# Kernel tuning notes

Measured on AMD Instinct MI355X. Metric: run time of the kernel, lower is better.

## Reference

```python
import jax, jax.numpy as jnp
import numpy as np

INPUT_SIZE = 63
HIDDEN = 128
NUM_CLASSES = 11
B, T = 4096, 128


def _gru_layer(x_seq, w_ih, w_hh, b_ih, b_hh):
    """PyTorch-semantics GRU layer. x_seq: [B,T,D] -> outputs [B,T,H]."""
    Bsz = x_seq.shape[0]
    H = w_hh.shape[1]
    # Precompute input projections for all timesteps in one big GEMM: [B,T,3H]
    gates_x = jnp.einsum('btd,gd->btg', x_seq, w_ih) + b_ih

    def step(h, gx):
        gh = h @ w_hh.T + b_hh                       # [B,3H]
        xr, xz, xn = jnp.split(gx, 3, axis=-1)
        hr, hz, hn = jnp.split(gh, 3, axis=-1)
        r = jax.nn.sigmoid(xr + hr)
        z = jax.nn.sigmoid(xz + hz)
        n = jnp.tanh(xn + r * hn)
        h_new = (1.0 - z) * n + z * h
        return h_new, h_new

    h0 = jnp.zeros((Bsz, H), x_seq.dtype)
    _, ys = jax.lax.scan(step, h0, jnp.swapaxes(gates_x, 0, 1))  # ys: [T,B,H]
    return jnp.swapaxes(ys, 0, 1)


def setup_inputs() -> dict:
    key = jax.random.key(0)
    ks = jax.random.split(key, 13)
    s_ih0 = 1.0 / np.sqrt(HIDDEN)
    u = lambda k, shape, s: jax.random.uniform(k, shape, jnp.float32, -s, s)
    inp = {
        'x': jax.random.normal(ks[0], (B, T, INPUT_SIZE), jnp.float32),
        # GRU layer 0: input_size=63 -> hidden=128
        'w_ih0': u(ks[1], (3 * HIDDEN, INPUT_SIZE), s_ih0),
        'w_hh0': u(ks[2], (3 * HIDDEN, HIDDEN), s_ih0),
        'b_ih0': u(ks[3], (3 * HIDDEN,), s_ih0),
        'b_hh0': u(ks[4], (3 * HIDDEN,), s_ih0),
        # GRU layer 1: hidden -> hidden
        'w_ih1': u(ks[5], (3 * HIDDEN, HIDDEN), s_ih0),
        'w_hh1': u(ks[6], (3 * HIDDEN, HIDDEN), s_ih0),
        'b_ih1': u(ks[7], (3 * HIDDEN,), s_ih0),
        'b_hh1': u(ks[8], (3 * HIDDEN,), s_ih0),
        # classifier: Linear(128,64) -> ReLU -> Linear(64,11)
        'w1': u(ks[9], (64, HIDDEN), 1.0 / np.sqrt(HIDDEN)),
        'b1': u(ks[10], (64,), 1.0 / np.sqrt(HIDDEN)),
        'w2': u(ks[11], (NUM_CLASSES, 64), 1.0 / np.sqrt(64)),
        'b2': u(ks[12], (NUM_CLASSES,), 1.0 / np.sqrt(64)),
    }
    return inp


def reference(x, w_ih0, w_hh0, b_ih0, b_hh0, w_ih1, w_hh1, b_ih1, b_hh1, w1, b1, w2, b2):
    h1 = _gru_layer(x, w_ih0, w_hh0, b_ih0, b_hh0)    # [B,T,H]
    h2 = _gru_layer(h1, w_ih1, w_hh1, b_ih1, b_hh1)   # [B,T,H]
    last = h2[:, -1, :]                               # [B,H]
    hidden = jax.nn.relu(last @ w1.T + b1)            # [B,64] (dropout is identity in eval)
    return hidden @ w2.T + b2                         # [B,num_classes]
```

## Files before the change

### kernel.cpp

```cpp
#include <hip/hip_runtime.h>
#include <hip/hip_bf16.h>

typedef __attribute__((ext_vector_type(8))) short s8v;
typedef __attribute__((ext_vector_type(4))) float f4v;

#define MF(A, B, C) C = __builtin_amdgcn_mfma_f32_16x16x32_bf16((A), (B), (C), 0, 0, 0)

__device__ __forceinline__ ushort f2bf(float f) {
  unsigned u = __float_as_uint(f);
  u += 0x7FFF + ((u >> 16) & 1);
  return (ushort)(u >> 16);
}
__device__ __forceinline__ float bf2f(ushort h) {
  return __uint_as_float(((unsigned)h) << 16);
}
__device__ __forceinline__ float sigm(float p) { return 1.f / (1.f + __expf(-p)); }
__device__ __forceinline__ float tanh_safe(float a) {
  float t = __expf(-2.f * fabsf(a));
  float ng = (1.f - t) / (1.f + t);
  return a < 0.f ? -ng : ng;
}
__device__ __forceinline__ float dot4(float4 a, float4 b) {
  return fmaf(a.x, b.x, fmaf(a.y, b.y, fmaf(a.z, b.z, a.w * b.w)));
}

__global__ void conv_x(const float* __restrict__ x, ushort* __restrict__ xhi,
                       ushort* __restrict__ xlo, int total) {
  int idx = blockIdx.x * 256 + threadIdx.x;
  if (idx >= total) return;
  int k4 = (idx & 15) * 4;
  long bt = idx >> 4;
  #pragma unroll
  for (int j = 0; j < 4; ++j) {
    int k = k4 + j;
    float v = (k < 63) ? x[bt * 63 + k] : 0.f;
    ushort hi = f2bf(v);
    xhi[bt * 64 + k] = hi;
    xlo[bt * 64 + k] = f2bf(v - bf2f(hi));
  }
}

__global__ void pack_fr(const float* __restrict__ src, ushort* __restrict__ dst,
                        int Kreal, int KT, int total) {
  int idx = blockIdx.x * 256 + threadIdx.x;
  if (idx >= total) return;
  int i = idx & 7, l = (idx >> 3) & 63, hl = (idx >> 9) & 1;
  int rest = idx >> 10;
  int kt = rest % KT, nt = rest / KT;
  int g = nt * 16 + (l & 15);
  int k = kt * 32 + (l >> 4) * 8 + i;
  float v = (k < Kreal) ? src[g * Kreal + k] : 0.f;
  ushort hi = f2bf(v);
  dst[idx] = hl ? f2bf(v - bf2f(hi)) : hi;
}

__global__ void __attribute__((amdgpu_flat_work_group_size(512, 512),
                               amdgpu_waves_per_eu(2, 2)))
rec_l0(const ushort* __restrict__ xhi, const ushort* __restrict__ xlo,
       const ushort* __restrict__ fih, const ushort* __restrict__ fhh,
       const float* __restrict__ bi, const float* __restrict__ bh,
       ushort* __restrict__ s_hi, ushort* __restrict__ s_lo,
       ushort* __restrict__ c_hi, ushort* __restrict__ c_lo,
       int t0, int tc, int first)
{
  __shared__ __align__(16) ushort hh_[2][2048], hl_[2][2048];
  __shared__ __align__(16) float bb[512];
  const int tid = threadIdx.x;
  const int l = tid & 63, wv = tid >> 6;
  const int lr = l & 15, lg = l >> 4;
  const long b0 = (long)blockIdx.x * 16;

  if (tid < 128) {
    bb[tid]       = bi[tid] + bh[tid];
    bb[128 + tid] = bi[128 + tid] + bh[128 + tid];
    bb[256 + tid] = bi[256 + tid];
    bb[384 + tid] = bh[256 + tid];
  }
  const int u0 = (wv << 4) + (lg << 2);
  const int hb = lr * 256 + ((u0 << 1) ^ ((lr & 7) << 4));
  if (first) {
    *(ushort4*)((char*)hh_[0] + hb) = make_ushort4(0, 0, 0, 0);
    *(ushort4*)((char*)hl_[0] + hb) = make_ushort4(0, 0, 0, 0);
  } else {
    *(ushort4*)((char*)hh_[0] + hb) = *(const ushort4*)&c_hi[(b0 + lr) * 128 + u0];
    *(ushort4*)((char*)hl_[0] + hb) = *(const ushort4*)&c_lo[(b0 + lr) * 128 + u0];
  }

  s8v Ba[12];
  s8v Bb[24];
  #pragma unroll
  for (int gi = 0; gi < 3; ++gi) {
    int nt = wv + 8 * gi;
    #pragma unroll
    for (int kt = 0; kt < 2; ++kt)
      #pragma unroll
      for (int hl = 0; hl < 2; ++hl)
        Ba[(gi * 2 + kt) * 2 + hl] = *(const s8v*)&fih[((long)((nt * 2 + kt) * 2 + hl)) * 512 + l * 8];
    #pragma unroll
    for (int kt = 0; kt < 4; ++kt)
      #pragma unroll
      for (int hl = 0; hl < 2; ++hl)
        Bb[(gi * 4 + kt) * 2 + hl] = *(const s8v*)&fhh[((long)((nt * 4 + kt) * 2 + hl)) * 512 + l * 8];
  }

  s8v xch[2], xcl[2], xnh[2], xnl[2];
  {
    long xo = ((b0 + lr) * 128 + t0) * 64 + lg * 8;
    xch[0] = *(const s8v*)&xhi[xo]; xch[1] = *(const s8v*)&xhi[xo + 32];
    xcl[0] = *(const s8v*)&xlo[xo]; xcl[1] = *(const s8v*)&xlo[xo + 32];
  }
  __syncthreads();

  const long sbase = (b0 + lr) * 128 + u0;
  ushort4 st_h, st_l;

  int pp = 0;
  for (int s = 0; s < tc; ++s, pp ^= 1) {
    if (s > 0) {
      *(ushort4*)&s_hi[sbase + (long)(s - 1) * 524288] = st_h;
      *(ushort4*)&s_lo[sbase + (long)(s - 1) * 524288] = st_l;
    }
    if (s + 1 < tc) {
      long xo = ((b0 + lr) * 128 + (t0 + s + 1)) * 64 + lg * 8;
      xnh[0] = *(const s8v*)&xhi[xo]; xnh[1] = *(const s8v*)&xhi[xo + 32];
      xnl[0] = *(const s8v*)&xlo[xo]; xnl[1] = *(const s8v*)&xlo[xo + 32];
    }
    f4v ar = {0.f, 0.f, 0.f, 0.f}, az = ar, anx = ar, anh = ar;
    #pragma unroll
    for (int kt = 0; kt < 4; ++kt) {
      int ba = lr * 256 + ((kt * 64 + lg * 16) ^ ((lr & 7) << 4));
      s8v Ah = *(const s8v*)((const char*)hh_[pp] + ba);
      s8v Al = *(const s8v*)((const char*)hl_[pp] + ba);
      MF(Bb[(0 * 4 + kt) * 2 + 0], Ah, ar);
      MF(Bb[(1 * 4 + kt) * 2 + 0], Ah, az);
      MF(Bb[(2 * 4 + kt) * 2 + 0], Ah, anh);
      MF(Bb[(0 * 4 + kt) * 2 + 1], Ah, ar);
      MF(Bb[(1 * 4 + kt) * 2 + 1], Ah, az);
      MF(Bb[(2 * 4 + kt) * 2 + 1], Ah, anh);
      MF(Bb[(0 * 4 + kt) * 2 + 0], Al, ar);
      MF(Bb[(1 * 4 + kt) * 2 + 0], Al, az);
      MF(Bb[(2 * 4 + kt) * 2 + 0], Al, anh);
    }
    #pragma unroll
    for (int kt = 0; kt < 2; ++kt) {
      MF(Ba[(0 * 2 + kt) * 2 + 0], xch[kt], ar);
      MF(Ba[(1 * 2 + kt) * 2 + 0], xch[kt], az);
      MF(Ba[(2 * 2 + kt) * 2 + 0], xch[kt], anx);
      MF(Ba[(0 * 2 + kt) * 2 + 1], xch[kt], ar);
      MF(Ba[(1 * 2 + kt) * 2 + 1], xch[kt], az);
      MF(Ba[(2 * 2 + kt) * 2 + 1], xch[kt], anx);
      MF(Ba[(0 * 2 + kt) * 2 + 0], xcl[kt], ar);
      MF(Ba[(1 * 2 + kt) * 2 + 0], xcl[kt], az);
      MF(Ba[(2 * 2 + kt) * 2 + 0], xcl[kt], anx);
    }
    {
      ushort4 oh = *(const ushort4*)((const char*)hh_[pp] + hb);
      ushort4 ol = *(const ushort4*)((const char*)hl_[pp] + hb);
      f4v vbr = *(const f4v*)&bb[u0];
      f4v vbz = *(const f4v*)&bb[128 + u0];
      f4v vbx = *(const f4v*)&bb[256 + u0];
      f4v vbh = *(const f4v*)&bb[384 + u0];
      const ushort* ohp = (const ushort*)&oh;
      const ushort* olp = (const ushort*)&ol;
      ushort nh_[4], nl_[4];
      #pragma unroll
      for (int j = 0; j < 4; ++j) {
        float hold = bf2f(ohp[j]) + bf2f(olp[j]);
        float rg = sigm(ar[j] + vbr[j]);
        float zg = sigm(az[j] + vbz[j]);
        float ng = tanh_safe(anx[j] + vbx[j] + rg * (anh[j] + vbh[j]));
        float hn = (1.f - zg) * ng + zg * hold;
        ushort hbf = f2bf(hn);
        nh_[j] = hbf; nl_[j] = f2bf(hn - bf2f(hbf));
      }
      ushort4 wh = make_ushort4(nh_[0], nh_[1], nh_[2], nh_[3]);
      ushort4 wl = make_ushort4(nl_[0], nl_[1], nl_[2], nl_[3]);
      *(ushort4*)((char*)hh_[pp ^ 1] + hb) = wh;
      *(ushort4*)((char*)hl_[pp ^ 1] + hb) = wl;
      st_h = wh; st_l = wl;
    }
    xch[0] = xnh[0]; xch[1] = xnh[1]; xcl[0] = xnl[0]; xcl[1] = xnl[1];
    __syncthreads();
  }
  *(ushort4*)&s_hi[sbase + (long)(tc - 1) * 524288] = st_h;
  *(ushort4*)&s_lo[sbase + (long)(tc - 1) * 524288] = st_l;
  *(ushort4*)&c_hi[(b0 + lr) * 128 + u0] = *(const ushort4*)((const char*)hh_[pp] + hb);
  *(ushort4*)&c_lo[(b0 + lr) * 128 + u0] = *(const ushort4*)((const char*)hl_[pp] + hb);
}

__global__ void __attribute__((amdgpu_flat_work_group_size(512, 512),
                               amdgpu_waves_per_eu(2, 2)))
rec_l1(const ushort* __restrict__ s_hi, const ushort* __restrict__ s_lo,
       const ushort* __restrict__ fih, const ushort* __restrict__ fhh,
       const float* __restrict__ bi, const float* __restrict__ bh,
       ushort* __restrict__ c_hi, ushort* __restrict__ c_lo,
       float* __restrict__ h1f, int tc, int first, int last)
{
  __shared__ __align__(16) ushort hh_[2][2048], hl_[2][2048];
  __shared__ __align__(16) ushort gh_[2][2048], gl_[2][2048];
  __shared__ __align__(16) float bb[512];
  const int tid = threadIdx.x;
  const int l = tid & 63, wv = tid >> 6;
  const int lr = l & 15, lg = l >> 4;
  const long b0 = (long)blockIdx.x * 16;

  if (tid < 128) {
    bb[tid]       = bi[tid] + bh[tid];
    bb[128 + tid] = bi[128 + tid] + bh[128 + tid];
    bb[256 + tid] = bi[256 + tid];
    bb[384 + tid] = bh[256 + tid];
  }
  const int u0 = (wv << 4) + (lg << 2);
  const int hb = lr * 256 + ((u0 << 1) ^ ((lr & 7) << 4));
  if (first) {
    *(ushort4*)((char*)hh_[0] + hb) = make_ushort4(0, 0, 0, 0);
    *(ushort4*)((char*)hl_[0] + hb) = make_ushort4(0, 0, 0, 0);
  } else {
    *(ushort4*)((char*)hh_[0] + hb) = *(const ushort4*)&c_hi[(b0 + lr) * 128 + u0];
    *(ushort4*)((char*)hl_[0] + hb) = *(const ushort4*)&c_lo[(b0 + lr) * 128 + u0];
  }

  const int stid = tid & 255;
  const int srow = stid >> 4, sc16 = stid & 15;
  const int sdst = srow * 256 + ((sc16 * 16) ^ ((srow & 7) << 4));
  const ushort* ssel = (tid < 256) ? s_hi : s_lo;
  ushort* dsel = (tid < 256) ? &gh_[0][0] : &gl_[0][0];

  s8v Ba[24], Bb[24];
  #pragma unroll
  for (int gi = 0; gi < 3; ++gi) {
    int nt = wv + 8 * gi;
    #pragma unroll
    for (int kt = 0; kt < 4; ++kt)
      #pragma unroll
      for (int hl = 0; hl < 2; ++hl) {
        Ba[(gi * 4 + kt) * 2 + hl] = *(const s8v*)&fih[((long)((nt * 4 + kt) * 2 + hl)) * 512 + l * 8];
        Bb[(gi * 4 + kt) * 2 + hl] = *(const s8v*)&fhh[((long)((nt * 4 + kt) * 2 + hl)) * 512 + l * 8];
      }
  }
  {
    s8v v = *(const s8v*)&ssel[((long)0 * 4096 + b0 + srow) * 128 + sc16 * 8];
    *(s8v*)((char*)(dsel + 0 * 2048) + sdst) = v;
  }
  __syncthreads();

  int pp = 0;
  for (int tl = 0; tl < tc; ++tl, pp ^= 1) {
    s8v sreg;
    const int havenext = (tl + 1 < tc);
    if (havenext)
      sreg = *(const s8v*)&ssel[((long)(tl + 1) * 4096 + b0 + srow) * 128 + sc16 * 8];

    f4v ar = {0.f, 0.f, 0.f, 0.f}, az = ar, anx = ar, anh = ar;
    #pragma unroll
    for (int kt = 0; kt < 4; ++kt) {
      int ba = lr * 256 + ((kt * 64 + lg * 16) ^ ((lr & 7) << 4));
      s8v Hh = *(const s8v*)((const char*)hh_[pp] + ba);
      s8v Hl = *(const s8v*)((const char*)hl_[pp] + ba);
      s8v Gh = *(const s8v*)((const char*)gh_[pp] + ba);
      s8v Gl = *(const s8v*)((const char*)gl_[pp] + ba);
      MF(Bb[(0 * 4 + kt) * 2 + 0], Hh, ar);
      MF(Ba[(0 * 4 + kt) * 2 + 0], Gh, ar);
      MF(Bb[(1 * 4 + kt) * 2 + 0], Hh, az);
      MF(Ba[(1 * 4 + kt) * 2 + 0], Gh, az);
      MF(Bb[(2 * 4 + kt) * 2 + 0], Hh, anh);
      MF(Ba[(2 * 4 + kt) * 2 + 0], Gh, anx);
      MF(Bb[(0 * 4 + kt) * 2 + 1], Hh, ar);
      MF(Ba[(0 * 4 + kt) * 2 + 1], Gh, ar);
      MF(Bb[(1 * 4 + kt) * 2 + 1], Hh, az);
      MF(Ba[(1 * 4 + kt) * 2 + 1], Gh, az);
      MF(Bb[(2 * 4 + kt) * 2 + 1], Hh, anh);
      MF(Ba[(2 * 4 + kt) * 2 + 1], Gh, anx);
      MF(Bb[(0 * 4 + kt) * 2 + 0], Hl, ar);
      MF(Ba[(0 * 4 + kt) * 2 + 0], Gl, ar);
      MF(Bb[(1 * 4 + kt) * 2 + 0], Hl, az);
      MF(Ba[(1 * 4 + kt) * 2 + 0], Gl, az);
      MF(Bb[(2 * 4 + kt) * 2 + 0], Hl, anh);
      MF(Ba[(2 * 4 + kt) * 2 + 0], Gl, anx);
    }
    {
      ushort4 oh = *(const ushort4*)((const char*)hh_[pp] + hb);
      ushort4 ol = *(const ushort4*)((const char*)hl_[pp] + hb);
      f4v vbr = *(const f4v*)&bb[u0];
      f4v vbz = *(const f4v*)&bb[128 + u0];
      f4v vbx = *(const f4v*)&bb[256 + u0];
      f4v vbh = *(const f4v*)&bb[384 + u0];
      const ushort* ohp = (const ushort*)&oh;
      const ushort* olp = (const ushort*)&ol;
      ushort nh_[4], nl_[4];
      #pragma unroll
      for (int j = 0; j < 4; ++j) {
        float hold = bf2f(ohp[j]) + bf2f(olp[j]);
        float rg = sigm(ar[j] + vbr[j]);
        float zg = sigm(az[j] + vbz[j]);
        float ng = tanh_safe(anx[j] + vbx[j] + rg * (anh[j] + vbh[j]));
        float hn = (1.f - zg) * ng + zg * hold;
        ushort hbf = f2bf(hn);
        nh_[j] = hbf; nl_[j] = f2bf(hn - bf2f(hbf));
      }
      *(ushort4*)((char*)hh_[pp ^ 1] + hb) = make_ushort4(nh_[0], nh_[1], nh_[2], nh_[3]);
      *(ushort4*)((char*)hl_[pp ^ 1] + hb) = make_ushort4(nl_[0], nl_[1], nl_[2], nl_[3]);
    }
    if (havenext)
      *(s8v*)((char*)(dsel + (size_t)(pp ^ 1) * 2048) + sdst) = sreg;
    __syncthreads();
  }
  {
    ushort4 fh = *(const ushort4*)((const char*)hh_[pp] + hb);
    ushort4 fl = *(const ushort4*)((const char*)hl_[pp] + hb);
    *(ushort4*)&c_hi[(b0 + lr) * 128 + u0] = fh;
    *(ushort4*)&c_lo[(b0 + lr) * 128 + u0] = fl;
    if (last) {
      const ushort* fhp = (const ushort*)&fh;
      const ushort* flp = (const ushort*)&fl;
      float4 o;
      o.x = bf2f(fhp[0]) + bf2f(flp[0]);
      o.y = bf2f(fhp[1]) + bf2f(flp[1]);
      o.z = bf2f(fhp[2]) + bf2f(flp[2]);
      o.w = bf2f(fhp[3]) + bf2f(flp[3]);
      *(float4*)&h1f[(b0 + lr) * 128 + u0] = o;
    }
  }
}

__global__ __launch_bounds__(512) void head_k(
    const float* __restrict__ h1f, const float* __restrict__ w1,
    const float* __restrict__ b1, const float* __restrict__ w2,
    const float* __restrict__ b2, float* __restrict__ out)
{
  __shared__ float hrow[16][132];
  __shared__ float w1s[64][132];
  __shared__ float hid[16][68];
  const int tid = threadIdx.x;
  const long b0 = (long)blockIdx.x * 16;
  for (int i = tid; i < 64 * 128; i += 512) w1s[i >> 7][i & 127] = w1[i];
  {
    int rr = tid >> 5, k4 = (tid & 31) * 4;
    *(float4*)&hrow[rr][k4] = *(const float4*)&h1f[(b0 + rr) * 128 + k4];
  }
  __syncthreads();
  {
    int r = tid & 15, fu = tid >> 4;
    float a0 = 0.f, a1 = 0.f;
    for (int k4 = 0; k4 < 32; ++k4) {
      float4 hv = *(const float4*)&hrow[r][k4 * 4];
      float4 wa = *(const float4*)&w1s[fu][k4 * 4];
      float4 wb = *(const float4*)&w1s[fu + 32][k4 * 4];
      a0 += dot4(wa, hv);
      a1 += dot4(wb, hv);
    }
    a0 += b1[fu]; a1 += b1[fu + 32];
    hid[r][fu]      = fmaxf(a0, 0.f);
    hid[r][fu + 32] = fmaxf(a1, 0.f);
  }
  __syncthreads();
  if (tid < 176) {
    int rr = tid / 11, c = tid - rr * 11;
    float acc = b2[c];
    for (int k = 0; k < 64; ++k) acc = fmaf(w2[c * 64 + k], hid[rr][k], acc);
    out[(b0 + rr) * 11 + c] = acc;
  }
}

extern "C" void kernel_launch(void* const* d_in, const int* in_sizes, int n_in,
                              void* d_out, int out_size, void* d_ws, size_t ws_size,
                              hipStream_t stream) {
  (void)in_sizes; (void)n_in; (void)out_size;
  const float* x    = (const float*)d_in[0];
  const float* wih0 = (const float*)d_in[1];
  const float* whh0 = (const float*)d_in[2];
  const float* bih0 = (const float*)d_in[3];
  const float* bhh0 = (const float*)d_in[4];
  const float* wih1 = (const float*)d_in[5];
  const float* whh1 = (const float*)d_in[6];
  const float* bih1 = (const float*)d_in[7];
  const float* bhh1 = (const float*)d_in[8];
  const float* w1   = (const float*)d_in[9];
  const float* b1   = (const float*)d_in[10];
  const float* w2   = (const float*)d_in[11];
  const float* b2   = (const float*)d_in[12];

  char* wsb = (char*)d_ws;
  size_t o = 0;
  ushort* fih0 = (ushort*)(wsb + o); o += 98304;
  ushort* fhh0 = (ushort*)(wsb + o); o += 196608;
  ushort* fih1 = (ushort*)(wsb + o); o += 196608;
  ushort* fhh1 = (ushort*)(wsb + o); o += 196608;
  ushort* xhi  = (ushort*)(wsb + o); o += 67108864ULL;
  ushort* xlo  = (ushort*)(wsb + o); o += 67108864ULL;
  ushort* hc0h = (ushort*)(wsb + o); o += 1048576;
  ushort* hc0l = (ushort*)(wsb + o); o += 1048576;
  ushort* hc1h = (ushort*)(wsb + o); o += 1048576;
  ushort* hc1l = (ushort*)(wsb + o); o += 1048576;
  float*  h1f  = (float*)(wsb + o);  o += 2097152;

  long rem = (long)ws_size - (long)o;
  long tcmax = rem / (2 * 1048576L);
  int Tc = tcmax > 128 ? 128 : (int)tcmax;
  if (Tc < 1) return;
  ushort* sh = (ushort*)(wsb + o);
  ushort* sl = sh + (long)Tc * 524288;

  hipLaunchKernelGGL(conv_x, dim3(32768), dim3(256), 0, stream, x, xhi, xlo, 8388608);
  hipLaunchKernelGGL(pack_fr, dim3(192), dim3(256), 0, stream, wih0, fih0, 63, 2, 49152);
  hipLaunchKernelGGL(pack_fr, dim3(384), dim3(256), 0, stream, whh0, fhh0, 128, 4, 98304);
  hipLaunchKernelGGL(pack_fr, dim3(384), dim3(256), 0, stream, wih1, fih1, 128, 4, 98304);
  hipLaunchKernelGGL(pack_fr, dim3(384), dim3(256), 0, stream, whh1, fhh1, 128, 4, 98304);

  for (int t0 = 0; t0 < 128; t0 += Tc) {
    int tc = (128 - t0) < Tc ? (128 - t0) : Tc;
    hipLaunchKernelGGL(rec_l0, dim3(256), dim3(512), 0, stream,
                       xhi, xlo, fih0, fhh0, bih0, bhh0, sh, sl, hc0h, hc0l,
                       t0, tc, (int)(t0 == 0));
    hipLaunchKernelGGL(rec_l1, dim3(256), dim3(512), 0, stream,
                       sh, sl, fih1, fhh1, bih1, bhh1, hc1h, hc1l, h1f,
                       tc, (int)(t0 == 0), (int)(t0 + tc == 128));
  }
  hipLaunchKernelGGL(head_k, dim3(256), dim3(512), 0, stream,
                     h1f, w1, b1, w2, b2, (float*)d_out);
}
```

Measured before the change: 652.6 us.

## Prefetch layer-1 inputs via global_load_lds and split MFMA accumulators

In the layer-1 GRU kernel, the next timestep's layer-0 output is now loaded straight into swizzled LDS with global_load_lds, replacing the register round-trip and explicit LDS store. In both recurrent kernels the r and z gate accumulators are split into separate input-path and hidden-path chains, which are summed at the gate. In the layer-0 kernel the input-projection MFMAs are issued before the hidden ones. The split breaks serial MFMA dependency chains so more instructions can be in flight, and the direct-to-LDS load frees registers and VALU work. The risk is the async LDS write ordering relative to the barrier, plus a few extra adds and accumulator registers.

Measured after the change: 703.1 us. +7.7%, slower.

```diff
diff --git a/kernel.cpp b/kernel.cpp
--- a/kernel.cpp
+++ b/kernel.cpp
@@ -22,6 +22,11 @@
 }
 __device__ __forceinline__ float dot4(float4 a, float4 b) {
   return fmaf(a.x, b.x, fmaf(a.y, b.y, fmaf(a.z, b.z, a.w * b.w)));
+}
+__device__ __forceinline__ void glds16(const ushort* g, ushort* l) {
+  __builtin_amdgcn_global_load_lds(
+      (const __attribute__((address_space(1))) unsigned int*)g,
+      (__attribute__((address_space(3))) unsigned int*)l, 16, 0, 0);
 }
 
 __global__ void conv_x(const float* __restrict__ x, ushort* __restrict__ xhi,
@@ -125,33 +130,34 @@
       xnh[0] = *(const s8v*)&xhi[xo]; xnh[1] = *(const s8v*)&xhi[xo + 32];
       xnl[0] = *(const s8v*)&xlo[xo]; xnl[1] = *(const s8v*)&xlo[xo + 32];
     }
-    f4v ar = {0.f, 0.f, 0.f, 0.f}, az = ar, anx = ar, anh = ar;
+    f4v arX = {0.f, 0.f, 0.f, 0.f}, azX = arX, anx = arX;
+    #pragma unroll
+    for (int kt = 0; kt < 2; ++kt) {
+      MF(Ba[(0 * 2 + kt) * 2 + 0], xch[kt], arX);
+      MF(Ba[(1 * 2 + kt) * 2 + 0], xch[kt], azX);
+      MF(Ba[(2 * 2 + kt) * 2 + 0], xch[kt], anx);
+      MF(Ba[(0 * 2 + kt) * 2 + 1], xch[kt], arX);
+      MF(Ba[(1 * 2 + kt) * 2 + 1], xch[kt], azX);
+      MF(Ba[(2 * 2 + kt) * 2 + 1], xch[kt], anx);
+      MF(Ba[(0 * 2 + kt) * 2 + 0], xcl[kt], arX);
+      MF(Ba[(1 * 2 + kt) * 2 + 0], xcl[kt], azX);
+      MF(Ba[(2 * 2 + kt) * 2 + 0], xcl[kt], anx);
+    }
+    f4v arH = {0.f, 0.f, 0.f, 0.f}, azH = arH, anh = arH;
     #pragma unroll
     for (int kt = 0; kt < 4; ++kt) {
       int ba = lr * 256 + ((kt * 64 + lg * 16) ^ ((lr & 7) << 4));
       s8v Ah = *(const s8v*)((const char*)hh_[pp] + ba);
       s8v Al = *(const s8v*)((const char*)hl_[pp] + ba);
-      MF(Bb[(0 * 4 + kt) * 2 + 0], Ah, ar);
-      MF(Bb[(1 * 4 + kt) * 2 + 0], Ah, az);
+      MF(Bb[(0 * 4 + kt) * 2 + 0], Ah, arH);
+      MF(Bb[(1 * 4 + kt) * 2 + 0], Ah, azH);
       MF(Bb[(2 * 4 + kt) * 2 + 0], Ah, anh);
-      MF(Bb[(0 * 4 + kt) * 2 + 1], Ah, ar);
-      MF(Bb[(1 * 4 + kt) * 2 + 1], Ah, az);
+      MF(Bb[(0 * 4 + kt) * 2 + 1], Ah, arH);
+      MF(Bb[(1 * 4 + kt) * 2 + 1], Ah, azH);
       MF(Bb[(2 * 4 + kt) * 2 + 1], Ah, anh);
-      MF(Bb[(0 * 4 + kt) * 2 + 0], Al, ar);
-      MF(Bb[(1 * 4 + kt) * 2 + 0], Al, az);
+      MF(Bb[(0 * 4 + kt) * 2 + 0], Al, arH);
+      MF(Bb[(1 * 4 + kt) * 2 + 0], Al, azH);
       MF(Bb[(2 * 4 + kt) * 2 + 0], Al, anh);
-    }
-    #pragma unroll
-    for (int kt = 0; kt < 2; ++kt) {
-      MF(Ba[(0 * 2 + kt) * 2 + 0], xch[kt], ar);
-      MF(Ba[(1 * 2 + kt) * 2 + 0], xch[kt], az);
-      MF(Ba[(2 * 2 + kt) * 2 + 0], xch[kt], anx);
-      MF(Ba[(0 * 2 + kt) * 2 + 1], xch[kt], ar);
-      MF(Ba[(1 * 2 + kt) * 2 + 1], xch[kt], az);
-      MF(Ba[(2 * 2 + kt) * 2 + 1], xch[kt], anx);
-      MF(Ba[(0 * 2 + kt) * 2 + 0], xcl[kt], ar);
-      MF(Ba[(1 * 2 + kt) * 2 + 0], xcl[kt], az);
-      MF(Ba[(2 * 2 + kt) * 2 + 0], xcl[kt], anx);
     }
     {
       ushort4 oh = *(const ushort4*)((const char*)hh_[pp] + hb);
@@ -166,8 +172,8 @@
       #pragma unroll
       for (int j = 0; j < 4; ++j) {
         float hold = bf2f(ohp[j]) + bf2f(olp[j]);
-        float rg = sigm(ar[j] + vbr[j]);
-        float zg = sigm(az[j] + vbz[j]);
+        float rg = sigm(arH[j] + arX[j] + vbr[j]);
+        float zg = sigm(azH[j] + azX[j] + vbz[j]);
         float ng = tanh_safe(anx[j] + vbx[j] + rg * (anh[j] + vbh[j]));
         float hn = (1.f - zg) * ng + zg * hold;
         ushort hbf = f2bf(hn);
@@ -220,11 +226,11 @@
     *(ushort4*)((char*)hl_[0] + hb) = *(const ushort4*)&c_lo[(b0 + lr) * 128 + u0];
   }
 
-  const int stid = tid & 255;
-  const int srow = stid >> 4, sc16 = stid & 15;
-  const int sdst = srow * 256 + ((sc16 * 16) ^ ((srow & 7) << 4));
-  const ushort* ssel = (tid < 256) ? s_hi : s_lo;
-  ushort* dsel = (tid < 256) ? &gh_[0][0] : &gl_[0][0];
+  const int spl = wv >> 2, srg = wv & 3;
+  const int srow = srg * 4 + (l >> 4);
+  const int swz_elem = ((l & 15) * 8) ^ ((srow & 7) << 3);
+  const ushort* ssel = spl ? s_lo : s_hi;
+  const long sgbase = (b0 + srow) * 128 + swz_elem;
 
   s8v Ba[24], Bb[24];
   #pragma unroll
@@ -239,19 +245,20 @@
       }
   }
   {
-    s8v v = *(const s8v*)&ssel[((long)0 * 4096 + b0 + srow) * 128 + sc16 * 8];
-    *(s8v*)((char*)(dsel + 0 * 2048) + sdst) = v;
+    ushort* ldst = (spl ? gl_[0] : gh_[0]) + srg * 512;
+    glds16(&ssel[sgbase], ldst);
   }
   __syncthreads();
 
   int pp = 0;
   for (int tl = 0; tl < tc; ++tl, pp ^= 1) {
-    s8v sreg;
-    const int havenext = (tl + 1 < tc);
-    if (havenext)
-      sreg = *(const s8v*)&ssel[((long)(tl + 1) * 4096 + b0 + srow) * 128 + sc16 * 8];
-
-    f4v ar = {0.f, 0.f, 0.f, 0.f}, az = ar, anx = ar, anh = ar;
+    if (tl + 1 < tc) {
+      ushort* ldst = (spl ? gl_[pp ^ 1] : gh_[pp ^ 1]) + srg * 512;
+      glds16(&ssel[(long)(tl + 1) * 524288 + sgbase], ldst);
+    }
+
+    f4v arH = {0.f, 0.f, 0.f, 0.f}, azH = arH, anh = arH;
+    f4v arG = arH, azG = arH, anx = arH;
     #pragma unroll
     for (int kt = 0; kt < 4; ++kt) {
       int ba = lr * 256 + ((kt * 64 + lg * 16) ^ ((lr & 7) << 4));
@@ -259,22 +266,22 @@
       s8v Hl = *(const s8v*)((const char*)hl_[pp] + ba);
       s8v Gh = *(const s8v*)((const char*)gh_[pp] + ba);
       s8v Gl = *(const s8v*)((const char*)gl_[pp] + ba);
-      MF(Bb[(0 * 4 + kt) * 2 + 0], Hh, ar);
-      MF(Ba[(0 * 4 + kt) * 2 + 0], Gh, ar);
-      MF(Bb[(1 * 4 + kt) * 2 + 0], Hh, az);
-      MF(Ba[(1 * 4 + kt) * 2 + 0], Gh, az);
+      MF(Bb[(0 * 4 + kt) * 2 + 0], Hh, arH);
+      MF(Ba[(0 * 4 + kt) * 2 + 0], Gh, arG);
+      MF(Bb[(1 * 4 + kt) * 2 + 0], Hh, azH);
+      MF(Ba[(1 * 4 + kt) * 2 + 0], Gh, azG);
       MF(Bb[(2 * 4 + kt) * 2 + 0], Hh, anh);
       MF(Ba[(2 * 4 + kt) * 2 + 0], Gh, anx);
-      MF(Bb[(0 * 4 + kt) * 2 + 1], Hh, ar);
-      MF(Ba[(0 * 4 + kt) * 2 + 1], Gh, ar);
-      MF(Bb[(1 * 4 + kt) * 2 + 1], Hh, az);
-      MF(Ba[(1 * 4 + kt) * 2 + 1], Gh, az);
+      MF(Bb[(0 * 4 + kt) * 2 + 1], Hh, arH);
+      MF(Ba[(0 * 4 + kt) * 2 + 1], Gh, arG);
+      MF(Bb[(1 * 4 + kt) * 2 + 1], Hh, azH);
+      MF(Ba[(1 * 4 + kt) * 2 + 1], Gh, azG);
       MF(Bb[(2 * 4 + kt) * 2 + 1], Hh, anh);
       MF(Ba[(2 * 4 + kt) * 2 + 1], Gh, anx);
-      MF(Bb[(0 * 4 + kt) * 2 + 0], Hl, ar);
-      MF(Ba[(0 * 4 + kt) * 2 + 0], Gl, ar);
-      MF(Bb[(1 * 4 + kt) * 2 + 0], Hl, az);
-      MF(Ba[(1 * 4 + kt) * 2 + 0], Gl, az);
+      MF(Bb[(0 * 4 + kt) * 2 + 0], Hl, arH);
+      MF(Ba[(0 * 4 + kt) * 2 + 0], Gl, arG);
+      MF(Bb[(1 * 4 + kt) * 2 + 0], Hl, azH);
+      MF(Ba[(1 * 4 + kt) * 2 + 0], Gl, azG);
       MF(Bb[(2 * 4 + kt) * 2 + 0], Hl, anh);
       MF(Ba[(2 * 4 + kt) * 2 + 0], Gl, anx);
     }
@@ -291,8 +298,8 @@
       #pragma unroll
       for (int j = 0; j < 4; ++j) {
         float hold = bf2f(ohp[j]) + bf2f(olp[j]);
-        float rg = sigm(ar[j] + vbr[j]);
-        float zg = sigm(az[j] + vbz[j]);
+        float rg = sigm(arH[j] + arG[j] + vbr[j]);
+        float zg = sigm(azH[j] + azG[j] + vbz[j]);
         float ng = tanh_safe(anx[j] + vbx[j] + rg * (anh[j] + vbh[j]));
         float hn = (1.f - zg) * ng + zg * hold;
         ushort hbf = f2bf(hn);
@@ -301,8 +308,6 @@
       *(ushort4*)((char*)hh_[pp ^ 1] + hb) = make_ushort4(nh_[0], nh_[1], nh_[2], nh_[3]);
       *(ushort4*)((char*)hl_[pp ^ 1] + hb) = make_ushort4(nl_[0], nl_[1], nl_[2], nl_[3]);
     }
-    if (havenext)
-      *(s8v*)((char*)(dsel + (size_t)(pp ^ 1) * 2048) + sdst) = sreg;
     __syncthreads();
   }
   {
```
